# Performance work log

Measured on AMD Instinct MI355X. Metric: run time of the kernel, lower is better.

The kernel has to match this reference:

```python
import jax, jax.numpy as jnp
import numpy as np

N_WIRES = 4
N_LAYERS = 4
N_PATCH = 14 * 14  # 196 2x2 patches of a 28x28 image


def _ry(state, theta, w):
    """Apply RY(theta) on wire w. state: (b, P, 2,2,2,2). theta: scalar or (b, P)."""
    ax = 2 + w
    s0 = jax.lax.slice_in_dim(state, 0, 1, axis=ax)
    s1 = jax.lax.slice_in_dim(state, 1, 2, axis=ax)
    c = jnp.cos(theta * 0.5)
    s = jnp.sin(theta * 0.5)
    if jnp.ndim(theta) > 0:  # per-(batch,patch) angles -> broadcast over wire axes
        c = c.reshape(c.shape + (1,) * N_WIRES)
        s = s.reshape(s.shape + (1,) * N_WIRES)
    return jnp.concatenate([c * s0 - s * s1, s * s0 + c * s1], axis=ax)


def _cx(state, ctrl, tgt):
    """Apply CNOT(ctrl, tgt): flip target axis on the ctrl=1 slice."""
    ca, ta = 2 + ctrl, 2 + tgt
    s0 = jax.lax.slice_in_dim(state, 0, 1, axis=ca)
    s1 = jnp.flip(jax.lax.slice_in_dim(state, 1, 2, axis=ca), axis=ta)
    return jnp.concatenate([s0, s1], axis=ca)


def setup_inputs() -> dict:
    key = jax.random.key(0)
    k1, k2, k3 = jax.random.split(key, 3)
    bsz = 8192
    x = jax.random.uniform(k1, (bsz, 784), dtype=jnp.float32)
    params = jax.random.normal(k2, (N_LAYERS, N_WIRES), dtype=jnp.float32)
    W = jax.random.normal(k3, (10, N_WIRES * N_PATCH), dtype=jnp.float32) * 0.03
    b = jnp.zeros((10,), dtype=jnp.float32)
    return {"x": x, "params": params, "W": W, "b": b}


def reference(x, params, W, b):
    bsz = x.shape[0]
    img = x.reshape(bsz, 28, 28)
    # 2x2 patches, row-major over (r, c), pixel order [r,c],[r,c+1],[r+1,c],[r+1,c+1]
    p = img.reshape(bsz, 14, 2, 14, 2).transpose(0, 1, 3, 2, 4).reshape(bsz, N_PATCH, 4)
    # |0000> state for every (batch, patch); all gates are real so real sim is exact
    state = jnp.zeros((bsz, N_PATCH, 2, 2, 2, 2), x.dtype).at[:, :, 0, 0, 0, 0].set(1.0)
    # encoder: RY(pixel) on each wire
    for w in range(N_WIRES):
        state = _ry(state, p[:, :, w], w)
    # ansatz: n_layers x (RY(param) per wire; CX(0,1); CX(2,3))
    for l in range(N_LAYERS):
        for w in range(N_WIRES):
            state = _ry(state, params[l, w], w)
        state = _cx(state, 0, 1)
        state = _cx(state, 2, 3)
    probs = state * state  # (b, P, 2,2,2,2)
    z = jnp.array([1.0, -1.0], x.dtype)  # PauliZ eigenvalues
    exp = jnp.stack([
        jnp.einsum('bpijkl,i->bp', probs, z),
        jnp.einsum('bpijkl,j->bp', probs, z),
        jnp.einsum('bpijkl,k->bp', probs, z),
        jnp.einsum('bpijkl,l->bp', probs, z),
    ], axis=-1)  # (b, P, 4), patch-major like torch.cat(patches, dim=1)
    feat = exp.reshape(bsz, N_PATCH * N_WIRES)
    logits = feat @ W.T + b
    return jax.nn.log_softmax(logits, axis=-1)
```

## Files before the change

kernel.cpp:

```cpp
#include <hip/hip_runtime.h>


#define RPB 4
#define NPIX 784
#define NPATCH 196

__device__ __forceinline__ float rfl(float v) {
    return __uint_as_float(__builtin_amdgcn_readfirstlane(__float_as_uint(v)));
}

__launch_bounds__(256, 8)
__global__ void quanv_kernel(const float* __restrict__ x,
                             const float* __restrict__ params,
                             const float* __restrict__ W,
                             const float* __restrict__ bias,
                             float* __restrict__ out,
                             int n_rows) {
    __shared__ __align__(16) float feat[RPB * NPIX];
    __shared__ float Ush[32];
    const int tid = threadIdx.x;
    const int row0 = blockIdx.x * RPB;

    if (tid < 8) {
        int pair = tid >> 2;
        int col  = tid & 3;
        float st[4];
#pragma unroll
        for (int i = 0; i < 4; ++i) st[i] = (i == col) ? 1.0f : 0.0f;
#pragma unroll
        for (int l = 0; l < 4; ++l) {
            float ah = 0.5f * params[l * 4 + pair * 2 + 0];
            float al = 0.5f * params[l * 4 + pair * 2 + 1];
            float ch = cosf(ah), sh = sinf(ah);
#pragma unroll
            for (int j = 0; j < 2; ++j) {
                float u = st[j], w = st[j + 2];
                st[j]     = ch * u - sh * w;
                st[j + 2] = sh * u + ch * w;
            }
            float cl = cosf(al), sl = sinf(al);
#pragma unroll
            for (int j = 0; j < 4; j += 2) {
                float u = st[j], w = st[j + 1];
                st[j]     = cl * u - sl * w;
                st[j + 1] = sl * u + cl * w;
            }
            float tmp = st[2]; st[2] = st[3]; st[3] = tmp;
        }
#pragma unroll
        for (int s = 0; s < 4; ++s) Ush[pair * 16 + s * 4 + col] = st[s];
    }
    __syncthreads();

    float Ua[16], Ub[16];
#pragma unroll
    for (int i = 0; i < 16; ++i) { Ua[i] = rfl(Ush[i]); Ub[i] = rfl(Ush[16 + i]); }

    for (int g = tid; g < RPB * NPATCH; g += 256) {
        int r = g / NPATCH;
        int P = g - r * NPATCH;
        int grow = row0 + r;
        float e0 = 0.f, e1 = 0.f, e2 = 0.f, e3 = 0.f;
        if (grow < n_rows) {
            int Pr = P / 14;
            int Pc = P - Pr * 14;
            const float* px = x + (size_t)grow * NPIX + Pr * 56 + Pc * 2;
            float2 t01 = *(const float2*)px;
            float2 t23 = *(const float2*)(px + 28);

            float c0 = __cosf(0.5f * t01.x), s0 = __sinf(0.5f * t01.x);
            float c1 = __cosf(0.5f * t01.y), s1 = __sinf(0.5f * t01.y);
            float c2 = __cosf(0.5f * t23.x), s2 = __sinf(0.5f * t23.x);
            float c3 = __cosf(0.5f * t23.y), s3 = __sinf(0.5f * t23.y);

            float pa[4] = { c0 * c1, c0 * s1, s0 * c1, s0 * s1 };
            float pb[4] = { c2 * c3, c2 * s3, s2 * c3, s2 * s3 };

            float qa[4], qb[4];
#pragma unroll
            for (int s = 0; s < 4; ++s) {
                float ya = fmaf(Ua[s * 4 + 3], pa[3],
                           fmaf(Ua[s * 4 + 2], pa[2],
                           fmaf(Ua[s * 4 + 1], pa[1], Ua[s * 4 + 0] * pa[0])));
                float yb = fmaf(Ub[s * 4 + 3], pb[3],
                           fmaf(Ub[s * 4 + 2], pb[2],
                           fmaf(Ub[s * 4 + 1], pb[1], Ub[s * 4 + 0] * pb[0])));
                qa[s] = ya * ya;
                qb[s] = yb * yb;
            }
            e0 = (qa[0] + qa[1]) - (qa[2] + qa[3]);
            e1 = (qa[0] - qa[1]) + (qa[2] - qa[3]);
            e2 = (qb[0] + qb[1]) - (qb[2] + qb[3]);
            e3 = (qb[0] - qb[1]) + (qb[2] - qb[3]);
        }
        *(float4*)&feat[r * NPIX + 4 * P] = make_float4(e0, e1, e2, e3);
    }
    __syncthreads();

    const int wid = tid >> 6, lane = tid & 63;
    const float4* W4 = (const float4*)W;
    for (int r = wid; r < RPB; r += 4) {
        int grow = row0 + r;
        if (grow >= n_rows) break;
        float acc[10];
#pragma unroll
        for (int o = 0; o < 10; ++o) acc[o] = 0.f;
        const float4* frow4 = (const float4*)&feat[r * NPIX];
        for (int k = lane; k < NPATCH; k += 64) {
            float4 f = frow4[k];
#pragma unroll
            for (int o = 0; o < 10; ++o) {
                float4 w = W4[o * NPATCH + k];
                acc[o] = fmaf(f.x, w.x, fmaf(f.y, w.y, fmaf(f.z, w.z, fmaf(f.w, w.w, acc[o]))));
            }
        }
#pragma unroll
        for (int o = 0; o < 10; ++o) {
            acc[o] += __shfl_xor(acc[o], 32, 64);
            acc[o] += __shfl_xor(acc[o], 16, 64);
            acc[o] += __shfl_xor(acc[o], 8, 64);
            acc[o] += __shfl_xor(acc[o], 4, 64);
            acc[o] += __shfl_xor(acc[o], 2, 64);
            acc[o] += __shfl_xor(acc[o], 1, 64);
        }
        if (lane == 0) {
            float lg[10], mx = -1e30f;
#pragma unroll
            for (int o = 0; o < 10; ++o) { lg[o] = acc[o] + bias[o]; mx = fmaxf(mx, lg[o]); }
            float sum = 0.f;
#pragma unroll
            for (int o = 0; o < 10; ++o) sum += __expf(lg[o] - mx);
            float lse = mx + __logf(sum);
#pragma unroll
            for (int o = 0; o < 10; ++o) out[(size_t)grow * 10 + o] = lg[o] - lse;
        }
    }
}

extern "C" void kernel_launch(void* const* d_in, const int* in_sizes, int n_in,
                              void* d_out, int out_size, void* d_ws, size_t ws_size,
                              hipStream_t stream) {
    const float* x      = (const float*)d_in[0];
    const float* params = (const float*)d_in[1];
    const float* W      = (const float*)d_in[2];
    const float* b      = (const float*)d_in[3];
    float* out = (float*)d_out;

    int n_rows = in_sizes[0] / NPIX;
    int nblocks = (n_rows + RPB - 1) / RPB;
    hipLaunchKernelGGL(quanv_kernel, dim3(nblocks), dim3(256), 0, stream,
                       x, params, W, b, out, n_rows);
}
```

Measured before the change: 85.97 us.

## Fuse feature computation into per-wave logits reduction and use hardware sin/cos

Each wavefront now owns one batch row and computes the patch expectation values straight into its 10 logit accumulators, dropping the shared-memory feature buffer and the block-wide barrier between the quantum-feature and linear stages. The per-pixel trig now uses the native amdgcn sin/cos intrinsics on a pre-scaled argument (revolutions, angle/(4π)) in place of __sinf/__cosf. This removes LDS traffic and a sync and frees LDS for occupancy. The cost is that each lane loops over four patch slots, with the last iteration partly idle.

```diff
diff --git a/kernel.cpp b/kernel.cpp
--- a/kernel.cpp
+++ b/kernel.cpp
@@ -4,6 +4,7 @@
 #define RPB 4
 #define NPIX 784
 #define NPATCH 196
+#define INV4PI 0.07957747154594767f
 
 __device__ __forceinline__ float rfl(float v) {
     return __uint_as_float(__builtin_amdgcn_readfirstlane(__float_as_uint(v)));
@@ -16,10 +17,8 @@
                              const float* __restrict__ bias,
                              float* __restrict__ out,
                              int n_rows) {
-    __shared__ __align__(16) float feat[RPB * NPIX];
     __shared__ float Ush[32];
     const int tid = threadIdx.x;
-    const int row0 = blockIdx.x * RPB;
 
     if (tid < 8) {
         int pair = tid >> 2;
@@ -56,84 +55,78 @@
 #pragma unroll
     for (int i = 0; i < 16; ++i) { Ua[i] = rfl(Ush[i]); Ub[i] = rfl(Ush[16 + i]); }
 
-    for (int g = tid; g < RPB * NPATCH; g += 256) {
-        int r = g / NPATCH;
-        int P = g - r * NPATCH;
-        int grow = row0 + r;
-        float e0 = 0.f, e1 = 0.f, e2 = 0.f, e3 = 0.f;
-        if (grow < n_rows) {
+    const int wid = tid >> 6, lane = tid & 63;
+    const int grow = blockIdx.x * RPB + wid;
+    if (grow >= n_rows) return;
+
+    const float* xrow = x + (size_t)grow * NPIX;
+    const float4* W4 = (const float4*)W;
+    float acc[10];
+#pragma unroll
+    for (int o = 0; o < 10; ++o) acc[o] = 0.f;
+
+#pragma unroll
+    for (int it = 0; it < 4; ++it) {
+        int P = lane + (it << 6);
+        if (P < NPATCH) {
             int Pr = P / 14;
             int Pc = P - Pr * 14;
-            const float* px = x + (size_t)grow * NPIX + Pr * 56 + Pc * 2;
-            float2 t01 = *(const float2*)px;
-            float2 t23 = *(const float2*)(px + 28);
+            const float* px = xrow + Pr * 56 + Pc * 2;
+            float2 top = *(const float2*)px;
+            float2 bot = *(const float2*)(px + 28);
 
-            float c0 = __cosf(0.5f * t01.x), s0 = __sinf(0.5f * t01.x);
-            float c1 = __cosf(0.5f * t01.y), s1 = __sinf(0.5f * t01.y);
-            float c2 = __cosf(0.5f * t23.x), s2 = __sinf(0.5f * t23.x);
-            float c3 = __cosf(0.5f * t23.y), s3 = __sinf(0.5f * t23.y);
+            float u;
+            u = top.x * INV4PI; float s0 = __builtin_amdgcn_sinf(u), c0 = __builtin_amdgcn_cosf(u);
+            u = top.y * INV4PI; float s1 = __builtin_amdgcn_sinf(u), c1 = __builtin_amdgcn_cosf(u);
+            u = bot.x * INV4PI; float s2 = __builtin_amdgcn_sinf(u), c2 = __builtin_amdgcn_cosf(u);
+            u = bot.y * INV4PI; float s3 = __builtin_amdgcn_sinf(u), c3 = __builtin_amdgcn_cosf(u);
 
-            float pa[4] = { c0 * c1, c0 * s1, s0 * c1, s0 * s1 };
-            float pb[4] = { c2 * c3, c2 * s3, s2 * c3, s2 * s3 };
-
+            float pa0 = c0 * c1, pa1 = c0 * s1, pa2 = s0 * c1, pa3 = s0 * s1;
+            float pb0 = c2 * c3, pb1 = c2 * s3, pb2 = s2 * c3, pb3 = s2 * s3;
             float qa[4], qb[4];
 #pragma unroll
             for (int s = 0; s < 4; ++s) {
-                float ya = fmaf(Ua[s * 4 + 3], pa[3],
-                           fmaf(Ua[s * 4 + 2], pa[2],
-                           fmaf(Ua[s * 4 + 1], pa[1], Ua[s * 4 + 0] * pa[0])));
-                float yb = fmaf(Ub[s * 4 + 3], pb[3],
-                           fmaf(Ub[s * 4 + 2], pb[2],
-                           fmaf(Ub[s * 4 + 1], pb[1], Ub[s * 4 + 0] * pb[0])));
+                float ya = fmaf(Ua[s * 4 + 3], pa3,
+                           fmaf(Ua[s * 4 + 2], pa2,
+                           fmaf(Ua[s * 4 + 1], pa1, Ua[s * 4 + 0] * pa0)));
+                float yb = fmaf(Ub[s * 4 + 3], pb3,
+                           fmaf(Ub[s * 4 + 2], pb2,
+                           fmaf(Ub[s * 4 + 1], pb1, Ub[s * 4 + 0] * pb0)));
                 qa[s] = ya * ya;
                 qb[s] = yb * yb;
             }
-            e0 = (qa[0] + qa[1]) - (qa[2] + qa[3]);
-            e1 = (qa[0] - qa[1]) + (qa[2] - qa[3]);
-            e2 = (qb[0] + qb[1]) - (qb[2] + qb[3]);
-            e3 = (qb[0] - qb[1]) + (qb[2] - qb[3]);
-        }
-        *(float4*)&feat[r * NPIX + 4 * P] = make_float4(e0, e1, e2, e3);
-    }
-    __syncthreads();
+            float e0 = (qa[0] + qa[1]) - (qa[2] + qa[3]);
+            float e1 = (qa[0] - qa[1]) + (qa[2] - qa[3]);
+            float e2 = (qb[0] + qb[1]) - (qb[2] + qb[3]);
+            float e3 = (qb[0] - qb[1]) + (qb[2] - qb[3]);
 
-    const int wid = tid >> 6, lane = tid & 63;
-    const float4* W4 = (const float4*)W;
-    for (int r = wid; r < RPB; r += 4) {
-        int grow = row0 + r;
-        if (grow >= n_rows) break;
-        float acc[10];
-#pragma unroll
-        for (int o = 0; o < 10; ++o) acc[o] = 0.f;
-        const float4* frow4 = (const float4*)&feat[r * NPIX];
-        for (int k = lane; k < NPATCH; k += 64) {
-            float4 f = frow4[k];
 #pragma unroll
             for (int o = 0; o < 10; ++o) {
-                float4 w = W4[o * NPATCH + k];
-                acc[o] = fmaf(f.x, w.x, fmaf(f.y, w.y, fmaf(f.z, w.z, fmaf(f.w, w.w, acc[o]))));
+                float4 w = W4[o * NPATCH + P];
+                acc[o] = fmaf(e0, w.x, fmaf(e1, w.y, fmaf(e2, w.z, fmaf(e3, w.w, acc[o]))));
             }
         }
+    }
+
 #pragma unroll
-        for (int o = 0; o < 10; ++o) {
-            acc[o] += __shfl_xor(acc[o], 32, 64);
-            acc[o] += __shfl_xor(acc[o], 16, 64);
-            acc[o] += __shfl_xor(acc[o], 8, 64);
-            acc[o] += __shfl_xor(acc[o], 4, 64);
-            acc[o] += __shfl_xor(acc[o], 2, 64);
-            acc[o] += __shfl_xor(acc[o], 1, 64);
-        }
-        if (lane == 0) {
-            float lg[10], mx = -1e30f;
+    for (int o = 0; o < 10; ++o) {
+        acc[o] += __shfl_xor(acc[o], 32, 64);
+        acc[o] += __shfl_xor(acc[o], 16, 64);
+        acc[o] += __shfl_xor(acc[o], 8, 64);
+        acc[o] += __shfl_xor(acc[o], 4, 64);
+        acc[o] += __shfl_xor(acc[o], 2, 64);
+        acc[o] += __shfl_xor(acc[o], 1, 64);
+    }
+    if (lane == 0) {
+        float lg[10], mx = -1e30f;
 #pragma unroll
-            for (int o = 0; o < 10; ++o) { lg[o] = acc[o] + bias[o]; mx = fmaxf(mx, lg[o]); }
-            float sum = 0.f;
+        for (int o = 0; o < 10; ++o) { lg[o] = acc[o] + bias[o]; mx = fmaxf(mx, lg[o]); }
+        float sum = 0.f;
 #pragma unroll
-            for (int o = 0; o < 10; ++o) sum += __expf(lg[o] - mx);
-            float lse = mx + __logf(sum);
+        for (int o = 0; o < 10; ++o) sum += __expf(lg[o] - mx);
+        float lse = mx + __logf(sum);
 #pragma unroll
-            for (int o = 0; o < 10; ++o) out[(size_t)grow * 10 + o] = lg[o] - lse;
-        }
+        for (int o = 0; o < 10; ++o) out[(size_t)grow * 10 + o] = lg[o] - lse;
     }
 }
 
```

Measured after the change: 114.1 us. 32.8% more time.
